# Performance work log

Hardware: AMD Instinct MI355X
Metric: run time of the kernel (lower is better)

The kernel has to match this reference:

```python
import jax, jax.numpy as jnp
import numpy as np

B, NS, NC, D = 32, 1024, 1024, 256   # batch, sentence len, comment len, latent/embedding dim
K = 128                              # co-attention latent size (self.k)
CLIP_R = 2.0
EPS = 1e-5

def _norm(x):
    return jnp.sqrt(jnp.maximum(jnp.sum(x * x, -1, keepdims=True), 1e-15))

def artanh(x):
    x = jnp.clip(x, -1 + 1e-5, 1 - 1e-5)
    return 0.5 * (jnp.log1p(x) - jnp.log1p(-x))

# ---------- Poincare ball, c = 1 ----------
def p_logmap0(y):
    yn = _norm(y)
    return artanh(yn) * y / yn

def p_expmap0(u):
    un = _norm(u)
    return jnp.tanh(un) * u / un

def mobius_add(x, y):
    xy = jnp.sum(x * y, -1, keepdims=True)
    x2 = jnp.sum(x * x, -1, keepdims=True)
    y2 = jnp.sum(y * y, -1, keepdims=True)
    num = (1 + 2 * xy + y2) * x + (1 - x2) * y
    den = jnp.maximum(1 + 2 * xy + x2 * y2, 1e-15)
    return num / den

def mobius_matvec(m, x):
    # geoopt convention: result = 'x @ m^T' transported through the ball
    xn = _norm(x)
    mx = jnp.matmul(x, jnp.swapaxes(m, -1, -2))
    mxn = _norm(mx)
    return jnp.tanh(mxn / xn * artanh(xn)) * mx / mxn

# ---------- Lorentz hyperboloid, k = 1 ----------
def l_expmap0_space(v_space):
    # exp map at origin of a tangent vector with zero time component
    vn = _norm(v_space)
    return jnp.concatenate([jnp.cosh(vn), jnp.sinh(vn) * v_space / vn], -1)

def euclid_to_lorentz(x):
    xn = _norm(x) + EPS
    x = x * jnp.minimum(1.0, CLIP_R / xn)  # clip_r feature clipping
    return l_expmap0_space(x)              # F.pad time=0 then expmap0

def lorentz_linear(x, W, b):
    y = jnp.matmul(x, W.T) + b
    space = y[..., 1:]
    time = jnp.sqrt(jnp.sum(space * space, -1, keepdims=True) + 1.0)
    return jnp.concatenate([time, space], -1)

def lorentz_act(x):
    space = jax.nn.gelu(x[..., 1:], approximate=False)
    time = jnp.sqrt(jnp.sum(space * space, -1, keepdims=True) + 1.0)
    return jnp.concatenate([time, space], -1)

def lorentz_to_poincare(x):
    return x[..., 1:] / (x[..., :1] + 1.0)

def l_inner(u, v):
    return -u[..., :1] * v[..., :1] + jnp.sum(u[..., 1:] * v[..., 1:], -1, keepdims=True)

def centroid(x, w):
    avg = jnp.matmul(w, x)  # weighted Lorentz average, then renormalize to hyperboloid
    den = jnp.sqrt(jnp.maximum(jnp.abs(l_inner(avg, avg)), 1e-8))
    return avg / den

def l_logmap0_space(x):
    t = jnp.maximum(x[..., :1], 1 + 1e-7)
    return jnp.arccosh(t) * x[..., 1:] / _norm(x[..., 1:])

def lorentz_concat(x, y):
    z = jnp.concatenate([l_logmap0_space(x), l_logmap0_space(y)], -1)
    return l_expmap0_space(z)


def setup_inputs() -> dict:
    key = jax.random.key(0)
    ks = jax.random.split(key, 8)
    sentence = jax.random.normal(ks[0], (B, NS, D), jnp.float32)
    comment = jax.random.normal(ks[1], (B, NC, D), jnp.float32)
    comment = 0.9 * comment / (_norm(comment) + 1.0)  # valid Poincare-ball points
    w = lambda k, o, i: jax.random.normal(k, (o, i), jnp.float32) * 0.05
    return {
        'sentence_rep': sentence,
        'comment_rep': comment,
        'Wl_W': w(ks[2], D + 1, D + 1), 'Wl_b': jnp.zeros((D + 1,), jnp.float32),
        'Wc_W': w(ks[3], K + 1, D + 1), 'Wc_b': jnp.zeros((K + 1,), jnp.float32),
        'Ws_W': w(ks[4], K + 1, D + 1), 'Ws_b': jnp.zeros((K + 1,), jnp.float32),
        'whs': jax.random.uniform(ks[5], (1, K), jnp.float32),
        'whc': jax.random.uniform(ks[6], (1, K), jnp.float32),
    }


def reference(sentence_rep, comment_rep, Wl_W, Wl_b, Wc_W, Wc_b, Ws_W, Ws_b, whs, whc):
    T = lambda a: jnp.swapaxes(a, -1, -2)
    # Fourier mixing (real part, as torch .float() on complex)
    s = jnp.fft.fft2(sentence_rep).real.astype(jnp.float32)
    c = jnp.fft.fft2(p_logmap0(comment_rep)).real.astype(jnp.float32)
    Ls = euclid_to_lorentz(s)            # [B,NS,D+1]
    Lc = euclid_to_lorentz(c)            # [B,NC,D+1]
    L = lorentz_linear(Lc, Wl_W, Wl_b)   # [B,NC,D+1]
    L = lorentz_act(jnp.einsum('bnd,bmd->bnm', Ls, L))  # [B,NS,NC] affinity
    # Ws(sentence) and Wc(comment) in Poincare coords (computed once; original recomputes)
    Hs_a = lorentz_to_poincare(lorentz_linear(Ls, Ws_W, Ws_b))  # [B,NS,K]
    Hc_a = lorentz_to_poincare(lorentz_linear(Lc, Wc_W, Wc_b))  # [B,NC,K]
    Hs_b = mobius_matvec(T(Hc_a), L)          # [B,NS,K]
    Hs = mobius_add(Hs_a, Hs_b)
    Hs = p_expmap0(jax.nn.gelu(p_logmap0(Hs), approximate=False))
    Hc_b = mobius_matvec(T(Hs_a), T(L))       # [B,NC,K]
    Hc = mobius_add(T(Hc_a), T(Hc_b))         # [B,K,NC]
    Hc = p_expmap0(jax.nn.gelu(p_logmap0(Hc), approximate=False))
    As = jax.nn.softmax(T(mobius_matvec(whs, Hs)), axis=-1)     # [B,1,NS]
    Ac = jax.nn.softmax(T(mobius_matvec(whc, T(Hc))), axis=-1)  # [B,1,NC]
    co_s = centroid(Ls, As)                   # [B,1,D+1]
    co_c = centroid(Lc, Ac)                   # [B,1,D+1]
    co_sc = jnp.squeeze(lorentz_concat(co_s, co_c), axis=1)     # [B,2D+1]
    return co_sc, As, Ac
```

## Files before the change

### kernel.cpp

```cpp
#include <hip/hip_runtime.h>
#include <cstdint>
#include <math.h>

#define NBATCH 32
#define NSQ 1024
#define NCQ 1024
#define DDIM 256
#define DP 257
#define KQ 128
#define KPAD 288
#define NFOLD 640
#define KF2 640
#define MXSPLIT 4194304

typedef __attribute__((ext_vector_type(8))) short short8;
typedef __attribute__((ext_vector_type(4))) float floatx4;

__device__ __forceinline__ float bf2f(ushort u) { return __uint_as_float(((uint)u) << 16); }
__device__ __forceinline__ ushort f2bf(float f) {
    uint u = __float_as_uint(f);
    return (ushort)((u + 0x7FFFu + ((u >> 16) & 1u)) >> 16);
}
__device__ __forceinline__ void gload16(const void* g, void* l) {
    __builtin_amdgcn_global_load_lds(
        (const __attribute__((address_space(1))) void*)g,
        (__attribute__((address_space(3))) void*)l,
        16, 0, 0);
}
__device__ __forceinline__ float artanh_clip(float x) {
    x = fminf(fmaxf(x, -1.0f + 1e-5f), 1.0f - 1e-5f);
    return 0.5f * (log1pf(x) - log1pf(-x));
}
__device__ __forceinline__ float gelu_f(float x) {
    return 0.5f * x * (1.0f + erff(x * 0.70710678118654752440f));
}
__device__ __forceinline__ float waveRedSum(float v) {
#pragma unroll
    for (int o = 32; o > 0; o >>= 1) v += __shfl_down(v, o, 64);
    return __shfl(v, 0, 64);
}
__device__ __forceinline__ void waveRedSum3(float& a, float& b, float& c) {
#pragma unroll
    for (int o = 32; o > 0; o >>= 1) {
        a += __shfl_down(a, o, 64);
        b += __shfl_down(b, o, 64);
        c += __shfl_down(c, o, 64);
    }
    a = __shfl(a, 0, 64); b = __shfl(b, 0, 64); c = __shfl(c, 0, 64);
}
__device__ __forceinline__ void waveRedSum2(float& a, float& b) {
#pragma unroll
    for (int o = 32; o > 0; o >>= 1) {
        a += __shfl_down(a, o, 64);
        b += __shfl_down(b, o, 64);
    }
    a = __shfl(a, 0, 64); b = __shfl(b, 0, 64);
}
__device__ __forceinline__ float blockRedSum(float v, float* buf) {
    int lane = threadIdx.x & 63, wid = threadIdx.x >> 6;
#pragma unroll
    for (int o = 32; o > 0; o >>= 1) v += __shfl_down(v, o, 64);
    __syncthreads();
    if (lane == 0) buf[wid] = v;
    __syncthreads();
    int nw = blockDim.x >> 6;
    float s = buf[0];
    for (int i = 1; i < nw; i++) s += buf[i];
    return s;
}
__device__ __forceinline__ float blockRedMax(float v, float* buf) {
    int lane = threadIdx.x & 63, wid = threadIdx.x >> 6;
#pragma unroll
    for (int o = 32; o > 0; o >>= 1) v = fmaxf(v, __shfl_down(v, o, 64));
    __syncthreads();
    if (lane == 0) buf[wid] = v;
    __syncthreads();
    int nw = blockDim.x >> 6;
    float s = buf[0];
    for (int i = 1; i < nw; i++) s = fmaxf(s, buf[i]);
    return s;
}

template <bool A_NN, bool B_NN, bool OUT_BF16, bool BIAS, bool ATOMIC, int NSPLIT, bool DUAL>
__global__ __launch_bounds__(256) void mfma_gemm(
    const short* __restrict__ A, int lda, int64_t sA,
    const short* __restrict__ B, int ldb, int64_t sB,
    void* __restrict__ Cv, int ldc, int64_t sC,
    const float* __restrict__ bias, int M, int N, int K,
    const short* __restrict__ A1, const short* __restrict__ B1, int64_t cOff1,
    const float* __restrict__ biasB)
{
    __shared__ short As[128][32];
    __shared__ short Bs[128][32];
    int bx = blockIdx.x, by = blockIdx.y, bz = blockIdx.z;
    {
        const int gx = gridDim.x, gy = gridDim.y;
        const int nblk = gx * gy * gridDim.z;
        if ((nblk & 7) == 0) {
            int flat = bx + gx * (by + gy * bz);
            int logical = (flat & 7) * (nblk >> 3) + (flat >> 3);
            bx = logical % gx; logical /= gx;
            by = logical % gy; bz = logical / gy;
        }
    }
    const int zz = bz;
    int zb, ks, half;
    if (DUAL) { half = zz & 1; zb = zz >> 1; ks = 0; }
    else      { zb = zz / NSPLIT; ks = zz - zb * NSPLIT; half = 0; }
    const short* Ap = (DUAL && half) ? A1 : A;
    const short* Bp = (DUAL && half) ? B1 : B;
    Ap += (int64_t)zb * sA;
    Bp += (int64_t)zb * sB;
    const int kper = K / NSPLIT;
    const int kbeg = ks * kper, kend = kbeg + kper;
    const int m0 = by * 128, n0 = bx * 128;
    const int t = threadIdx.x;
    const int lane = t & 63, w = t >> 6;
    const int wm = (w & 1) * 64, wn = (w >> 1) * 64;
    floatx4 acc[4][4] = {};
    for (int k0 = kbeg; k0 < kend; k0 += 32) {
        if (!A_NN) {
            int r = t >> 2, c8 = (t & 3) * 8;
            const short* ap = Ap + (int64_t)(m0 + r) * lda + k0 + c8;
            gload16(ap, &As[r][c8]);
            gload16(ap + (int64_t)64 * lda, &As[r + 64][c8]);
        } else {
            int r2 = t >> 4, c8 = (t & 15) * 8;
            int kk = 2 * r2;
            const ushort* a0 = (const ushort*)Ap + (int64_t)(k0 + kk) * lda + m0 + c8;
            uint4 v0 = *(const uint4*)a0;
            uint4 v1 = *(const uint4*)(a0 + lda);
            const ushort* p0 = (const ushort*)&v0;
            const ushort* p1 = (const ushort*)&v1;
#pragma unroll
            for (int i = 0; i < 8; i++) {
                uint pk = (uint)p0[i] | ((uint)p1[i] << 16);
                *(uint*)&As[c8 + i][kk] = pk;
            }
        }
        if (!B_NN) {
            int r = t >> 2, c8 = (t & 3) * 8;
            const short* bp = Bp + (int64_t)(n0 + r) * ldb + k0 + c8;
            gload16(bp, &Bs[r][c8]);
            gload16(bp + (int64_t)64 * ldb, &Bs[r + 64][c8]);
        } else {
            int r2 = t >> 4, c8 = (t & 15) * 8;
            int kk = 2 * r2;
            const ushort* b0 = (const ushort*)Bp + (int64_t)(k0 + kk) * ldb + n0 + c8;
            uint4 v0 = *(const uint4*)b0;
            uint4 v1 = *(const uint4*)(b0 + ldb);
            const ushort* p0 = (const ushort*)&v0;
            const ushort* p1 = (const ushort*)&v1;
#pragma unroll
            for (int i = 0; i < 8; i++) {
                uint pk = (uint)p0[i] | ((uint)p1[i] << 16);
                *(uint*)&Bs[c8 + i][kk] = pk;
            }
        }
        __syncthreads();
        short8 af[4], bfv[4];
#pragma unroll
        for (int i = 0; i < 4; i++)
            af[i] = *(const short8*)&As[wm + 16 * i + (lane & 15)][8 * (lane >> 4)];
#pragma unroll
        for (int i = 0; i < 4; i++)
            bfv[i] = *(const short8*)&Bs[wn + 16 * i + (lane & 15)][8 * (lane >> 4)];
#pragma unroll
        for (int i = 0; i < 4; i++)
#pragma unroll
            for (int j = 0; j < 4; j++)
                acc[i][j] = __builtin_amdgcn_mfma_f32_16x16x32_bf16(af[i], bfv[j], acc[i][j], 0, 0, 0);
        __syncthreads();
    }
    const int q = lane >> 4, c = lane & 15;
    int64_t cbase = (int64_t)zb * sC + ((DUAL && half) ? cOff1 : 0);
    if (NSPLIT > 1 && !ATOMIC) cbase += (int64_t)ks * cOff1;
    const float* bsel = (BIAS && biasB && zb) ? biasB : bias;
#pragma unroll
    for (int j = 0; j < 4; j++) {
        int col = n0 + wn + 16 * j + c;
        float bv = BIAS ? bsel[col] : 0.0f;
#pragma unroll
        for (int i = 0; i < 4; i++) {
            int rowb = m0 + wm + 16 * i + 4 * q;
#pragma unroll
            for (int r = 0; r < 4; r++) {
                float v = acc[i][j][r] + bv;
                int64_t idx = cbase + (int64_t)(rowb + r) * ldc + col;
                if (ATOMIC)       atomicAdd((float*)Cv + idx, v);
                else if (OUT_BF16) ((ushort*)Cv)[idx] = f2bf(v);
                else               ((float*)Cv)[idx] = v;
            }
        }
    }
}

__global__ __launch_bounds__(256) void genconst_kernel(
    ushort* CS1c, ushort* CS1s, ushort* C2, ushort* S2,
    const float* __restrict__ WlW, const float* __restrict__ WsW, const float* __restrict__ WcW,
    ushort* Wl, ushort* Ws, ushort* Wc)
{
    int blk = blockIdx.x, t = threadIdx.x;
    if (blk < 3200) {
        int idx = blk * 256 + t;
        int hs = idx >= 409600;
        int e = idx - hs * 409600;
        int n = e / KF2, k = e - n * KF2;
        float v = 0.0f;
        if (k <= 512) {
            int p = (n * k) & 1023;
            float ang = (6.28318530717958647692f / 1024.0f) * (float)p;
            v = hs ? ((k == 0) ? 0.0f : -sinf(ang)) : cosf(ang);
        }
        (hs ? CS1s : CS1c)[e] = f2bf(v);
    } else if (blk < 3456) {
        int idx = (blk - 3200) * 256 + t;
        int d = idx >> 8, j = idx & 255;
        int p = (d * j) & 255;
        float ang = (6.28318530717958647692f / 256.0f) * (float)p;
        C2[idx] = f2bf(cosf(ang));
        S2[idx] = f2bf(sinf(ang));
    } else {
        int r = blk - 3456;
        const float* src; ushort* dst; int srow;
        if (r < 256)      { src = WlW; dst = Wl + r * KPAD;        srow = r + 1; }
        else if (r < 384) { src = WsW; dst = Ws + (r - 256) * KPAD; srow = r - 256 + 1; }
        else              { src = WcW; dst = Wc + (r - 384) * KPAD; srow = r - 384 + 1; }
        dst[t] = (t < DP) ? f2bf(src[(int64_t)srow * DP + t]) : (ushort)0;
        if (t < KPAD - 256) {
            int t2 = t + 256;
            dst[t2] = (t2 < DP) ? f2bf(src[(int64_t)srow * DP + t2]) : (ushort)0;
        }
    }
}

__global__ __launch_bounds__(256) void prep_fold_kernel(const float* __restrict__ sent,
                                                        const float* __restrict__ comm,
                                                        ushort* __restrict__ XC, ushort* __restrict__ XS) {
    int bp = blockIdx.x;
    int z = blockIdx.y * 4 + (threadIdx.x >> 6);
    int lane = threadIdx.x & 63;
    int m2 = (1024 - bp) & 1023;
    const float* base = (z < 32) ? sent + (int64_t)z * 262144 : comm + (int64_t)(z - 32) * 262144;
    float4 a = *(const float4*)(base + bp * 256 + 4 * lane);
    float4 b = *(const float4*)(base + m2 * 256 + 4 * lane);
    if (z >= 32) {
        float s1 = a.x * a.x + a.y * a.y + a.z * a.z + a.w * a.w;
        float s2 = b.x * b.x + b.y * b.y + b.z * b.z + b.w * b.w;
        waveRedSum2(s1, s2);
        float yn1 = sqrtf(fmaxf(s1, 1e-15f));
        float f1 = artanh_clip(yn1) / yn1;
        a.x *= f1; a.y *= f1; a.z *= f1; a.w *= f1;
        float yn2 = sqrtf(fmaxf(s2, 1e-15f));
        float f2v = artanh_clip(yn2) / yn2;
        b.x *= f2v; b.y *= f2v; b.z *= f2v; b.w *= f2v;
    }
    int64_t o = ((int64_t)z * NFOLD + bp) * 256 + 4 * lane;
    bool single = (bp == 0) || (bp == 512);
    ushort4 oc;
    oc.x = f2bf(single ? a.x : a.x + b.x);
    oc.y = f2bf(single ? a.y : a.y + b.y);
    oc.z = f2bf(single ? a.z : a.z + b.z);
    oc.w = f2bf(single ? a.w : a.w + b.w);
    *(ushort4*)(XC + o) = oc;
    if (!single) {
        ushort4 os;
        os.x = f2bf(a.x - b.x); os.y = f2bf(a.y - b.y);
        os.z = f2bf(a.z - b.z); os.w = f2bf(a.w - b.w);
        *(ushort4*)(XS + o) = os;
    }
}

__global__ __launch_bounds__(256) void e2l_kernel(const ushort* __restrict__ YcYs,
                                                  ushort* __restrict__ Lsb, ushort* __restrict__ Lcb) {
    int64_t row = (int64_t)blockIdx.x * 4 + (threadIdx.x >> 6);
    int lane = threadIdx.x & 63;
    int z = (int)(row >> 10), n = (int)(row & 1023);
    int np = (n <= 512) ? n : 1024 - n;
    float sgn = (n <= 512) ? 1.0f : -1.0f;
    const ushort* base = YcYs + (int64_t)z * 327680 + np * 256 + 4 * lane;
    ushort4 uc = *(const ushort4*)base;
    ushort4 us = *(const ushort4*)(base + 163840);
    float v0 = bf2f(uc.x) + sgn * bf2f(us.x);
    float v1 = bf2f(uc.y) + sgn * bf2f(us.y);
    float v2 = bf2f(uc.z) + sgn * bf2f(us.z);
    float v3 = bf2f(uc.w) + sgn * bf2f(us.w);
    float s = waveRedSum(v0 * v0 + v1 * v1 + v2 * v2 + v3 * v3);
    float xn = sqrtf(fmaxf(s, 1e-15f)) + 1e-5f;
    float sc = fminf(1.0f, 2.0f / xn);
    float s2 = fmaxf(s * sc * sc, 1e-15f);
    float vn = sqrtf(s2);
    float e = expf(vn);
    float ei = 1.0f / e;
    float shv = (vn < 1e-4f) ? 1.0f : (e - ei) * 0.5f / vn;
    float fac = shv * sc;
    ushort* ob = (row < 32768 ? Lsb + row * KPAD : Lcb + (row - 32768) * KPAD);
    ob[1 + 4 * lane + 0] = f2bf(fac * v0);
    ob[1 + 4 * lane + 1] = f2bf(fac * v1);
    ob[1 + 4 * lane + 2] = f2bf(fac * v2);
    ob[1 + 4 * lane + 3] = f2bf(fac * v3);
    if (lane == 0) ob[0] = f2bf((e + ei) * 0.5f);
    if (lane < KPAD - DP) ob[DP + lane] = 0;
}

__global__ __launch_bounds__(256) void lnorm_kernel(ushort* __restrict__ Llin_bf) {
    int64_t row = (int64_t)blockIdx.x * 4 + (threadIdx.x >> 6);
    int lane = threadIdx.x & 63;
    ushort* ob = Llin_bf + row * KPAD;
    float s = 0.f;
#pragma unroll
    for (int i = 0; i < 4; i++) { float v = bf2f(ob[1 + 4 * lane + i]); s += v * v; }
    s = waveRedSum(s);
    if (lane == 0) ob[0] = f2bf(sqrtf(s + 1.0f));
    if (lane < KPAD - DP) ob[DP + lane] = 0;
}

__global__ __launch_bounds__(256) void poinc2_kernel(ushort* __restrict__ Hcat) {
    int64_t row = (int64_t)blockIdx.x * 4 + (threadIdx.x >> 6);
    int lane = threadIdx.x & 63;
    ushort* r = Hcat + row * KQ;
    ushort2 u = *(ushort2*)&r[2 * lane];
    float v0 = bf2f(u.x), v1 = bf2f(u.y);
    float s = waveRedSum(v0 * v0 + v1 * v1);
    float inv = 1.0f / (sqrtf(s + 1.0f) + 1.0f);
    ushort2 o; o.x = f2bf(v0 * inv); o.y = f2bf(v1 * inv);
    *(ushort2*)&r[2 * lane] = o;
}

__global__ __launch_bounds__(256) void tmat_kernel(ushort* __restrict__ inout, ushort* __restrict__ outp,
                                                   float* __restrict__ rowpart, float* __restrict__ colpart) {
    __shared__ ushort tile[64][68];
    int z = blockIdx.z;
    int r0 = blockIdx.x * 64, c0 = blockIdx.y * 64;
    ushort* ib = inout + (int64_t)z * 1048576;
    ushort* ob = outp + (int64_t)z * 1048576;
    int t = threadIdx.x;
    int row = t >> 2;
    int cq = (t & 3) * 8;
    {
        ushort* src = ib + (int64_t)(r0 + row) * 1024 + c0;
        float rsum = 0.f;
#pragma unroll
        for (int s = 0; s < 2; s++) {
            int cb = cq + 32 * s;
            uint4 v = *(const uint4*)(src + cb);
            ushort g[8];
            const ushort* pv = (const ushort*)&v;
#pragma unroll
            for (int k = 0; k < 8; k++) {
                g[k] = f2bf(gelu_f(bf2f(pv[k])));
                float fb = bf2f(g[k]);
                if (!(c0 == 0 && cb == 0 && k == 0)) rsum += fb * fb;
            }
            *(uint4*)(src + cb) = *(const uint4*)g;
            *(ushort4*)&tile[row][cb] = *(const ushort4*)&g[0];
            *(ushort4*)&tile[row][cb + 4] = *(const ushort4*)&g[4];
        }
        rsum += __shfl_xor(rsum, 1, 64);
        rsum += __shfl_xor(rsum, 2, 64);
        if ((t & 3) == 0)
            rowpart[((int64_t)(z * 16 + blockIdx.y)) * 1024 + r0 + row] = rsum;
    }
    __syncthreads();
    {
        int i2 = row;
        ushort* dst = ob + (int64_t)(c0 + i2) * 1024 + r0;
        float csum = 0.f;
#pragma unroll
        for (int s = 0; s < 2; s++) {
            int cb = cq + 32 * s;
            ushort g[8];
#pragma unroll
            for (int k = 0; k < 8; k++) {
                g[k] = tile[cb + k][i2];
                float a = bf2f(g[k]);
                csum += a * a;
            }
            *(uint4*)(dst + cb) = *(const uint4*)g;
        }
        csum += __shfl_xor(csum, 1, 64);
        csum += __shfl_xor(csum, 2, 64);
        if ((t & 3) == 0)
            colpart[((int64_t)(z * 16 + blockIdx.x)) * 1024 + c0 + i2] = csum;
    }
}

__global__ __launch_bounds__(256) void combine_kernel(
    const float* __restrict__ rowpart, const float* __restrict__ colpart,
    ushort* __restrict__ Lmat, ushort* __restrict__ LmatT,
    float* __restrict__ xnrow, float* __restrict__ colsum)
{
    __shared__ float red[4];
    int b = blockIdx.x, t = threadIdx.x;
    float t2 = 0.f;
#pragma unroll
    for (int i = 0; i < 4; i++) {
        int n = t + 256 * i;
        const float* rp = rowpart + (int64_t)b * 16384 + n;
        float s = 0.f;
#pragma unroll
        for (int c = 0; c < 16; c++) s += rp[c * 1024];
        float tim = sqrtf(1.0f + s);
        ushort tb = f2bf(tim);
        Lmat[((int64_t)(b * 1024 + n)) * 1024] = tb;
        LmatT[(int64_t)b * 1048576 + n] = tb;
        xnrow[b * 1024 + n] = sqrtf(fmaxf(1.0f + 2.0f * s, 1e-15f));
        t2 += tim * tim;
    }
#pragma unroll
    for (int i = 0; i < 4; i++) {
        int m = t + 256 * i;
        const float* cp = colpart + (int64_t)b * 16384 + m;
        float s = 0.f;
#pragma unroll
        for (int c = 0; c < 16; c++) s += cp[c * 1024];
        if (m > 0) colsum[b * 1024 + m] = s;
    }
    float tt = blockRedSum(t2, red);
    if (t == 0) colsum[b * 1024] = tt;
}

__global__ __launch_bounds__(256) void colfac_kernel(const float* __restrict__ colsum,
                                                     const float* __restrict__ mxcT,
                                                     float* __restrict__ fac_c) {
    int b = blockIdx.x; int m = blockIdx.y * 256 + threadIdx.x;
    float xn = sqrtf(fmaxf(colsum[b * NCQ + m], 1e-15f));
    const float* base = mxcT + (int64_t)b * KQ * NCQ + m;
    const float* base2 = base + MXSPLIT;
    float sm = 0.f;
    for (int j = 0; j < KQ; j++) {
        float v = base[j * NCQ] + base2[j * NCQ];
        sm += v * v;
    }
    float mxn = sqrtf(fmaxf(sm, 1e-15f));
    fac_c[b * NCQ + m] = tanhf(mxn / xn * artanh_clip(xn)) / mxn;
}

__global__ __launch_bounds__(256) void rowops_s_kernel(
    const ushort* __restrict__ Hsa, const float* __restrict__ mxs,
    const float* __restrict__ xnrow, const float* __restrict__ whs,
    float* __restrict__ logits)
{
    const int t = threadIdx.x;
    const int lane = t & 63;
    const int wid = t >> 6;
    const int sub = lane & 7;
    const int rg  = lane >> 3;
    const int64_t row = (int64_t)blockIdx.x * 32 + wid * 8 + rg;
    const ushort* p = Hsa + row * KQ + sub * 16;
    const float*  q = mxs + row * KQ + sub * 16;

    float pf[16], qf[16];
    {
        uint4 u0 = *(const uint4*)p;
        uint4 u1 = *(const uint4*)(p + 8);
        const ushort* pu0 = (const ushort*)&u0;
        const ushort* pu1 = (const ushort*)&u1;
#pragma unroll
        for (int i = 0; i < 8; i++) { pf[i] = bf2f(pu0[i]); pf[8 + i] = bf2f(pu1[i]); }
    }
#pragma unroll
    for (int i = 0; i < 16; i += 4) {
        float4 a  = *(const float4*)(q + i);
        float4 b2 = *(const float4*)(q + i + MXSPLIT);
        qf[i + 0] = a.x + b2.x; qf[i + 1] = a.y + b2.y;
        qf[i + 2] = a.z + b2.z; qf[i + 3] = a.w + b2.w;
    }
    float r1 = 0.f, r2 = 0.f, r3 = 0.f;
#pragma unroll
    for (int i = 0; i < 16; i++) {
        r1 += qf[i] * qf[i]; r2 += pf[i] * qf[i]; r3 += pf[i] * pf[i];
    }
#pragma unroll
    for (int o = 4; o > 0; o >>= 1) {
        r1 += __shfl_xor(r1, o, 64);
        r2 += __shfl_xor(r2, o, 64);
        r3 += __shfl_xor(r3, o, 64);
    }
    float mxn = sqrtf(fmaxf(r1, 1e-15f));
    float xn = xnrow[row];
    float fac = tanhf(mxn / xn * artanh_clip(xn)) / mxn;
    float xy = fac * r2;
    float x2 = r3;
    float y2 = fac * fac * r1;
    float ca = 1.f + 2.f * xy + y2, cb = 1.f - x2;
    float den = fmaxf(1.f + 2.f * xy + x2 * y2, 1e-15f);
    float hn2 = (ca * ca * x2 + 2.f * ca * cb * xy + cb * cb * y2) / (den * den);
    float hn = sqrtf(fmaxf(hn2, 1e-15f));
    float uf = artanh_clip(hn) / hn;
    float ufd = uf / den;
    float cbf = cb * fac;
    float wv[16];
#pragma unroll
    for (int i = 0; i < 16; i += 4) *(float4*)&wv[i] = *(const float4*)(whs + sub * 16 + i);
    float r4 = 0.f, r5 = 0.f;
#pragma unroll
    for (int i = 0; i < 16; i++) {
        float g = gelu_f(ufd * (ca * pf[i] + cbf * qf[i]));
        r4 += g * g;
        r5 += g * wv[i];
    }
#pragma unroll
    for (int o = 4; o > 0; o >>= 1) {
        r4 += __shfl_xor(r4, o, 64);
        r5 += __shfl_xor(r5, o, 64);
    }
    float gn = sqrtf(fmaxf(r4, 1e-15f));
    float ef = tanhf(gn) / gn;
    float dot = ef * r5;
    float Hn = sqrtf(fmaxf(ef * ef * r4, 1e-15f));
    float mxn2 = sqrtf(fmaxf(dot * dot, 1e-15f));
    float lg = tanhf(mxn2 / Hn * artanh_clip(Hn)) * dot / mxn2;
    if (sub == 0) logits[row] = lg;
}

__global__ void thsa_kernel(const ushort* __restrict__ in, ushort* __restrict__ outp) {
    __shared__ ushort tile[32][33];
    int z = blockIdx.z;
    int n0 = blockIdx.x * 32, j0 = blockIdx.y * 32;
    const ushort* ib = in + (int64_t)z * 131072;
    ushort* ob = outp + (int64_t)z * 131072;
    int tx = threadIdx.x, ty = threadIdx.y;
    for (int i = 0; i < 32; i += 8) tile[ty + i][tx] = ib[(n0 + ty + i) * 128 + j0 + tx];
    __syncthreads();
    for (int i = 0; i < 32; i += 8) ob[(j0 + ty + i) * 1024 + n0 + tx] = tile[tx][ty + i];
}

__global__ __launch_bounds__(256) void rowops_c_kernel(const ushort* __restrict__ HcAT,
                                                       float* __restrict__ mx,
                                                       const float* __restrict__ fac_c) {
    int64_t row = (int64_t)blockIdx.x * 4 + (threadIdx.x >> 6);
    int lane = threadIdx.x & 63;
    int b = (int)(row >> 7);
    const ushort* xb = HcAT + row * (int64_t)NCQ + 16 * lane;
    float* yb = mx + row * (int64_t)NCQ + 16 * lane;
    const float* fb = fac_c + b * NCQ + 16 * lane;
    float xv[16], yv[16];
    {
        uint4 u0 = *(const uint4*)xb;
        uint4 u1 = *(const uint4*)(xb + 8);
        const ushort* pu0 = (const ushort*)&u0;
        const ushort* pu1 = (const ushort*)&u1;
#pragma unroll
        for (int i = 0; i < 8; i++) { xv[i] = bf2f(pu0[i]); xv[8 + i] = bf2f(pu1[i]); }
    }
#pragma unroll
    for (int i = 0; i < 16; i += 4) {
        float4 v1 = *(const float4*)(yb + i);
        float4 v2 = *(const float4*)(yb + i + MXSPLIT);
        float4 fv = *(const float4*)(fb + i);
        yv[i + 0] = fv.x * (v1.x + v2.x);
        yv[i + 1] = fv.y * (v1.y + v2.y);
        yv[i + 2] = fv.z * (v1.z + v2.z);
        yv[i + 3] = fv.w * (v1.w + v2.w);
    }
    float xy = 0.f, x2 = 0.f, y2 = 0.f;
#pragma unroll
    for (int i = 0; i < 16; i++) { xy += xv[i] * yv[i]; x2 += xv[i] * xv[i]; y2 += yv[i] * yv[i]; }
    waveRedSum3(xy, x2, y2);
    float ca = 1.f + 2.f * xy + y2, cb = 1.f - x2;
    float den = fmaxf(1.f + 2.f * xy + x2 * y2, 1e-15f);
    float hn2 = (ca * ca * x2 + 2.f * ca * cb * xy + cb * cb * y2) / (den * den);
    float hn = sqrtf(fmaxf(hn2, 1e-15f));
    float uf = artanh_clip(hn) / hn;
    float g[16]; float gn2 = 0.f;
#pragma unroll
    for (int i = 0; i < 16; i++) {
        float h = (ca * xv[i] + cb * yv[i]) / den;
        g[i] = gelu_f(uf * h);
        gn2 += g[i] * g[i];
    }
    gn2 = waveRedSum(gn2);
    float gn = sqrtf(fmaxf(gn2, 1e-15f));
    float ef = tanhf(gn) / gn;
#pragma unroll
    for (int i = 0; i < 16; i += 4) {
        float4 o = {ef * g[i], ef * g[i + 1], ef * g[i + 2], ef * g[i + 3]};
        *(float4*)(yb + i) = o;
    }
}

__global__ __launch_bounds__(256) void logitsc_kernel(const float* __restrict__ Hc, const float* __restrict__ whc, float* __restrict__ lgc) {
    int b = blockIdx.x; int m = blockIdx.y * 256 + threadIdx.x;
    const float* base = Hc + (int64_t)b * KQ * NCQ + m;
    float s1 = 0.f, s2 = 0.f;
    for (int j = 0; j < KQ; j++) { float v = base[j * NCQ]; s1 += v * whc[j]; s2 += v * v; }
    float xn = sqrtf(fmaxf(s2, 1e-15f));
    float mxn = sqrtf(fmaxf(s1 * s1, 1e-15f));
    lgc[b * NCQ + m] = tanhf(mxn / xn * artanh_clip(xn)) * s1 / mxn;
}

__global__ __launch_bounds__(256) void softmax_kernel(const float* __restrict__ lg, float* __restrict__ outp) {
    __shared__ float red[4];
    int b = blockIdx.x; int t = threadIdx.x;
    const float* x = lg + b * 1024;
    float v[4]; float m = -1e30f;
#pragma unroll
    for (int i = 0; i < 4; i++) { v[i] = x[t + 256 * i]; m = fmaxf(m, v[i]); }
    m = blockRedMax(m, red);
    float s = 0.f;
#pragma unroll
    for (int i = 0; i < 4; i++) { v[i] = expf(v[i] - m); s += v[i]; }
    s = blockRedSum(s, red);
    float inv = 1.0f / s;
#pragma unroll
    for (int i = 0; i < 4; i++) outp[b * 1024 + t + 256 * i] = v[i] * inv;
}

__global__ __launch_bounds__(320) void centroidA_kernel(
    const ushort* __restrict__ Lsb, const ushort* __restrict__ Lcb,
    const float* __restrict__ As, const float* __restrict__ Ac,
    float* __restrict__ part)
{
    int b = blockIdx.x;
    int which = blockIdx.y;
    int chunk = blockIdx.z;
    const ushort* L = which ? Lcb : Lsb;
    const float* w = which ? Ac : As;
    int t = threadIdx.x;
    if (t >= DP) return;
    const ushort* Lb = L + (int64_t)b * NSQ * KPAD + (int64_t)chunk * 128 * KPAD + t;
    const float* wb = w + b * NSQ + chunk * 128;
    float s = 0.f;
    for (int n = 0; n < 128; n++) s += wb[n] * bf2f(Lb[(int64_t)n * KPAD]);
    part[((int64_t)((b * 2 + which) * 8 + chunk)) * 264 + t] = s;
}
__global__ __launch_bounds__(320) void centroidB_kernel(
    const float* __restrict__ part, float* __restrict__ co_s, float* __restrict__ co_c)
{
    int b = blockIdx.x;
    int which = blockIdx.y;
    int t = threadIdx.x;
    if (t >= DP) return;
    const float* p = part + (int64_t)(b * 2 + which) * 8 * 264 + t;
    float s = 0.f;
#pragma unroll
    for (int c = 0; c < 8; c++) s += p[c * 264];
    (which ? co_c : co_s)[b * DP + t] = s;
}

__global__ __launch_bounds__(256) void final_kernel(const float* __restrict__ co_s, const float* __restrict__ co_c, float* __restrict__ outp) {
    __shared__ float red[4];
    int b = blockIdx.x, t = threadIdx.x;
    float zmine[2];
    for (int w = 0; w < 2; w++) {
        const float* co = (w ? co_c : co_s) + b * DP;
        float at = co[0];
        float asp = co[1 + t];
        float ssp = blockRedSum(asp * asp, red);
        float li = ssp - at * at;
        float den = sqrtf(fmaxf(fabsf(li), 1e-8f));
        float xt = at / den, xsp = asp / den;
        float s2 = blockRedSum(xsp * xsp, red);
        float nrm = sqrtf(fmaxf(s2, 1e-15f));
        float ac = acoshf(fmaxf(xt, 1.0f + 1e-7f));
        zmine[w] = ac * xsp / nrm;
    }
    float vn2 = blockRedSum(zmine[0] * zmine[0] + zmine[1] * zmine[1], red);
    float vn = sqrtf(fmaxf(vn2, 1e-15f));
    float sc = sinhf(vn) / vn;
    if (t == 0) outp[b * 513] = coshf(vn);
    outp[b * 513 + 1 + t] = sc * zmine[0];
    outp[b * 513 + 1 + 256 + t] = sc * zmine[1];
}

extern "C" void kernel_launch(void* const* d_in, const int* in_sizes, int n_in,
                              void* d_out, int out_size, void* d_ws, size_t ws_size,
                              hipStream_t stream)
{
    const float* sent = (const float*)d_in[0];
    const float* comm = (const float*)d_in[1];
    const float* WlW  = (const float*)d_in[2];
    const float* Wlb  = (const float*)d_in[3];
    const float* WcW  = (const float*)d_in[4];
    const float* Wcb  = (const float*)d_in[5];
    const float* WsW  = (const float*)d_in[6];
    const float* Wsb  = (const float*)d_in[7];
    const float* whs  = (const float*)d_in[8];
    const float* whc  = (const float*)d_in[9];
    float* out = (float*)d_out;
    (void)in_sizes; (void)n_in; (void)out_size; (void)ws_size;

    float* ws = (float*)d_ws;
    size_t off = 0;
    auto take = [&](size_t n) { float* p = ws + off; off += n; return p; };
    float*  xnrow = take(32768);
    float*  fac_c = take(32768);
    float*  lgs   = take(32768);
    float*  lgc   = take(32768);
    float*  co_s  = take(8224);
    float*  co_c  = take(8224);
    ushort* Ls_bf = (ushort*)take(4718592);
    ushort* Lc_bf = (ushort*)take(4718592);
    ushort* Wl_bf = (ushort*)take(36864);
    ushort* Ws_bf = (ushort*)take(18432);
    ushort* Wc_bf = (ushort*)take(18432);
    ushort* HsA_bf = (ushort*)take(2097152);
    ushort* HcA_bf = (ushort*)take(2097152);
    float*  part_cn   = take(1048576);
    float*  part_cent = take(135168);
    ushort* LmatT_bf  = (ushort*)take(16777216);
    float*  F     = take(33554432);

    ushort* XC_bf   = (ushort*)F;
    ushort* XS_bf   = (ushort*)(F + 5242880);
    ushort* Ff_bf   = (ushort*)(F + 10485760);
    ushort* CS1c    = (ushort*)(F + 20971520);
    ushort* CS1s    = (ushort*)(F + 21176320);
    ushort* C2_bf   = (ushort*)(F + 21381120);
    ushort* S2_bf   = (ushort*)(F + 21413888);
    ushort* YcYs    = (ushort*)F;
    ushort* Lmat_bf = (ushort*)F;
    ushort* Llin_bf = (ushort*)(F + 29360128);
    float*  mx      = F + 16777216;
    ushort* HsAT    = (ushort*)(F + 25165824);
    ushort* HcAT    = (ushort*)(F + 27262976);
    float*  colpart = F + 29360128;
    float*  colsum  = F + 30408704;

    float* AsOut = out + 16416;
    float* AcOut = out + 16416 + 32768;

    dim3 blk(256);
    const short* NUL = nullptr;

    genconst_kernel<<<3968, 256, 0, stream>>>(CS1c, CS1s, C2_bf, S2_bf, WlW, WsW, WcW, Wl_bf, Ws_bf, Wc_bf);

    prep_fold_kernel<<<dim3(513, 16), blk, 0, stream>>>(sent, comm, XC_bf, XS_bf);
    mfma_gemm<false,false,true,false,false,1,true><<<dim3(5,2,128), blk, 0, stream>>>(
        (const short*)C2_bf,256,0, (const short*)XC_bf,256,(int64_t)NFOLD*256, Ff_bf,1280,(int64_t)256*1280,
        nullptr, 256,NFOLD,256, (const short*)S2_bf, (const short*)XS_bf, 640, nullptr);
    mfma_gemm<false,false,true,false,false,1,true><<<dim3(2,5,128), blk, 0, stream>>>(
        (const short*)CS1c,KF2,0, (const short*)Ff_bf,1280,(int64_t)256*1280, YcYs,256,327680,
        nullptr, NFOLD,256,544, (const short*)CS1s, (const short*)(Ff_bf+640), 163840, nullptr);
    e2l_kernel<<<16384, blk, 0, stream>>>(YcYs, Ls_bf, Lc_bf);

    mfma_gemm<false,false,true,true,false,1,false><<<dim3(2,256,1), blk, 0, stream>>>(
        (const short*)Lc_bf,KPAD,0, (const short*)Wl_bf,KPAD,0, (void*)(Llin_bf+1),KPAD,0,
        Wlb+1, 32768,256,KPAD, NUL, NUL, 0, nullptr);
    lnorm_kernel<<<8192, blk, 0, stream>>>(Llin_bf);

    mfma_gemm<false,false,true,false,false,1,false><<<dim3(8,8,32), blk, 0, stream>>>(
        (const short*)Ls_bf,KPAD,294912, (const short*)Llin_bf,KPAD,294912, Lmat_bf,1024,1048576,
        nullptr, 1024,1024,KPAD, NUL, NUL, 0, nullptr);
    tmat_kernel<<<dim3(16,16,32), blk, 0, stream>>>(Lmat_bf, LmatT_bf, part_cn, colpart);
    combine_kernel<<<32, blk, 0, stream>>>(part_cn, colpart, Lmat_bf, LmatT_bf, xnrow, colsum);

    mfma_gemm<false,false,true,true,false,1,false><<<dim3(1,256,2), blk, 0, stream>>>(
        (const short*)Ls_bf,KPAD,9437184, (const short*)Ws_bf,KPAD,36864, HsA_bf,128,4194304,
        Wsb+1, 32768,128,KPAD, NUL, NUL, 0, Wcb+1);
    poinc2_kernel<<<16384, blk, 0, stream>>>(HsA_bf);

    thsa_kernel<<<dim3(32,4,64), dim3(32,8), 0, stream>>>(HsA_bf, HsAT);

    mfma_gemm<false,false,false,false,false,2,false><<<dim3(1,8,64), blk, 0, stream>>>(
        (const short*)Lmat_bf,1024,1048576, (const short*)HcAT,1024,131072, mx,128,131072,
        nullptr, 1024,128,1024, NUL, NUL, MXSPLIT, nullptr);
    rowops_s_kernel<<<1024, blk, 0, stream>>>(HsA_bf, mx, xnrow, whs, lgs);

    mfma_gemm<false,false,false,false,false,2,false><<<dim3(8,1,64), blk, 0, stream>>>(
        (const short*)HsAT,1024,131072, (const short*)LmatT_bf,1024,1048576, mx,1024,131072,
        nullptr, 128,1024,1024, NUL, NUL, MXSPLIT, nullptr);
    colfac_kernel<<<dim3(32,4), blk, 0, stream>>>(colsum, mx, fac_c);
    rowops_c_kernel<<<1024, blk, 0, stream>>>(HcAT, mx, fac_c);
    logitsc_kernel<<<dim3(32,4), blk, 0, stream>>>(mx, whc, lgc);

    softmax_kernel<<<64, blk, 0, stream>>>(lgs, AsOut);
    centroidA_kernel<<<dim3(32,2,8), 320, 0, stream>>>(Ls_bf, Lc_bf, AsOut, AcOut, part_cent);
    centroidB_kernel<<<dim3(32,2), 320, 0, stream>>>(part_cent, co_s, co_c);
    final_kernel<<<32, blk, 0, stream>>>(co_s, co_c, out);
}
```

Before: 468.0 us.

## Process two K-slices per barrier in GEMM and table-drive DFT constant generation

The MFMA GEMM now stages two 32-wide K tiles into separate LDS buffers before a single barrier pair and runs both MFMA batches. This halves barrier count per K step and gives more loads in flight, at the cost of doubled LDS per block, which may reduce occupancy. The unused NN transpose-load paths are removed. Constant generation now precomputes a 1024-entry cos/sin table once and uses lookups in restructured per-row blocks instead of per-element sinf/cosf across thousands of blocks.

```diff
diff --git a/kernel.cpp b/kernel.cpp
--- a/kernel.cpp
+++ b/kernel.cpp
@@ -81,7 +81,7 @@
     return s;
 }
 
-template <bool A_NN, bool B_NN, bool OUT_BF16, bool BIAS, bool ATOMIC, int NSPLIT, bool DUAL>
+template <bool OUT_BF16, bool BIAS, bool ATOMIC, int NSPLIT, bool DUAL>
 __global__ __launch_bounds__(256) void mfma_gemm(
     const short* __restrict__ A, int lda, int64_t sA,
     const short* __restrict__ B, int ldb, int64_t sB,
@@ -90,8 +90,10 @@
     const short* __restrict__ A1, const short* __restrict__ B1, int64_t cOff1,
     const float* __restrict__ biasB)
 {
-    __shared__ short As[128][32];
-    __shared__ short Bs[128][32];
+    __shared__ short As0[128][32];
+    __shared__ short Bs0[128][32];
+    __shared__ short As1[128][32];
+    __shared__ short Bs1[128][32];
     int bx = blockIdx.x, by = blockIdx.y, bz = blockIdx.z;
     {
         const int gx = gridDim.x, gy = gridDim.y;
@@ -117,61 +119,50 @@
     const int t = threadIdx.x;
     const int lane = t & 63, w = t >> 6;
     const int wm = (w & 1) * 64, wn = (w >> 1) * 64;
+    const int sr = t >> 2, sc8 = (t & 3) * 8;
     floatx4 acc[4][4] = {};
-    for (int k0 = kbeg; k0 < kend; k0 += 32) {
-        if (!A_NN) {
-            int r = t >> 2, c8 = (t & 3) * 8;
-            const short* ap = Ap + (int64_t)(m0 + r) * lda + k0 + c8;
-            gload16(ap, &As[r][c8]);
-            gload16(ap + (int64_t)64 * lda, &As[r + 64][c8]);
-        } else {
-            int r2 = t >> 4, c8 = (t & 15) * 8;
-            int kk = 2 * r2;
-            const ushort* a0 = (const ushort*)Ap + (int64_t)(k0 + kk) * lda + m0 + c8;
-            uint4 v0 = *(const uint4*)a0;
-            uint4 v1 = *(const uint4*)(a0 + lda);
-            const ushort* p0 = (const ushort*)&v0;
-            const ushort* p1 = (const ushort*)&v1;
-#pragma unroll
-            for (int i = 0; i < 8; i++) {
-                uint pk = (uint)p0[i] | ((uint)p1[i] << 16);
-                *(uint*)&As[c8 + i][kk] = pk;
-            }
-        }
-        if (!B_NN) {
-            int r = t >> 2, c8 = (t & 3) * 8;
-            const short* bp = Bp + (int64_t)(n0 + r) * ldb + k0 + c8;
-            gload16(bp, &Bs[r][c8]);
-            gload16(bp + (int64_t)64 * ldb, &Bs[r + 64][c8]);
-        } else {
-            int r2 = t >> 4, c8 = (t & 15) * 8;
-            int kk = 2 * r2;
-            const ushort* b0 = (const ushort*)Bp + (int64_t)(k0 + kk) * ldb + n0 + c8;
-            uint4 v0 = *(const uint4*)b0;
-            uint4 v1 = *(const uint4*)(b0 + ldb);
-            const ushort* p0 = (const ushort*)&v0;
-            const ushort* p1 = (const ushort*)&v1;
-#pragma unroll
-            for (int i = 0; i < 8; i++) {
-                uint pk = (uint)p0[i] | ((uint)p1[i] << 16);
-                *(uint*)&Bs[c8 + i][kk] = pk;
-            }
-        }
-        __syncthreads();
+
+    auto stageA = [&](short (*S)[32], int kk) {
+        const short* ap = Ap + (int64_t)(m0 + sr) * lda + kk + sc8;
+        gload16(ap, &S[sr][sc8]);
+        gload16(ap + (int64_t)64 * lda, &S[sr + 64][sc8]);
+    };
+    auto stageB = [&](short (*S)[32], int kk) {
+        const short* bp = Bp + (int64_t)(n0 + sr) * ldb + kk + sc8;
+        gload16(bp, &S[sr][sc8]);
+        gload16(bp + (int64_t)64 * ldb, &S[sr + 64][sc8]);
+    };
+    auto domfma = [&](short (*SA)[32], short (*SB)[32]) {
         short8 af[4], bfv[4];
 #pragma unroll
         for (int i = 0; i < 4; i++)
-            af[i] = *(const short8*)&As[wm + 16 * i + (lane & 15)][8 * (lane >> 4)];
+            af[i] = *(const short8*)&SA[wm + 16 * i + (lane & 15)][8 * (lane >> 4)];
 #pragma unroll
         for (int i = 0; i < 4; i++)
-            bfv[i] = *(const short8*)&Bs[wn + 16 * i + (lane & 15)][8 * (lane >> 4)];
+            bfv[i] = *(const short8*)&SB[wn + 16 * i + (lane & 15)][8 * (lane >> 4)];
 #pragma unroll
         for (int i = 0; i < 4; i++)
 #pragma unroll
             for (int j = 0; j < 4; j++)
                 acc[i][j] = __builtin_amdgcn_mfma_f32_16x16x32_bf16(af[i], bfv[j], acc[i][j], 0, 0, 0);
+    };
+
+    int k0 = kbeg;
+    for (; k0 + 64 <= kend; k0 += 64) {
+        stageA(As0, k0);       stageB(Bs0, k0);
+        stageA(As1, k0 + 32);  stageB(Bs1, k0 + 32);
         __syncthreads();
-    }
+        domfma(As0, Bs0);
+        domfma(As1, Bs1);
+        __syncthreads();
+    }
+    if (k0 < kend) {
+        stageA(As0, k0);      stageB(Bs0, k0);
+        __syncthreads();
+        domfma(As0, Bs0);
+        __syncthreads();
+    }
+
     const int q = lane >> 4, c = lane & 15;
     int64_t cbase = (int64_t)zb * sC + ((DUAL && half) ? cOff1 : 0);
     if (NSPLIT > 1 && !ATOMIC) cbase += (int64_t)ks * cOff1;
@@ -195,33 +186,49 @@
     }
 }
 
+__global__ __launch_bounds__(256) void trigtab_kernel(float* __restrict__ tab) {
+    int p = blockIdx.x * 256 + threadIdx.x;
+    float ang = (6.28318530717958647692f / 1024.0f) * (float)p;
+    tab[p] = cosf(ang);
+    tab[1024 + p] = sinf(ang);
+}
+
 __global__ __launch_bounds__(256) void genconst_kernel(
+    const float* __restrict__ tab,
     ushort* CS1c, ushort* CS1s, ushort* C2, ushort* S2,
     const float* __restrict__ WlW, const float* __restrict__ WsW, const float* __restrict__ WcW,
     ushort* Wl, ushort* Ws, ushort* Wc)
 {
+    __shared__ float lct[1024], lst[1024];
     int blk = blockIdx.x, t = threadIdx.x;
-    if (blk < 3200) {
-        int idx = blk * 256 + t;
-        int hs = idx >= 409600;
-        int e = idx - hs * 409600;
-        int n = e / KF2, k = e - n * KF2;
-        float v = 0.0f;
-        if (k <= 512) {
-            int p = (n * k) & 1023;
-            float ang = (6.28318530717958647692f / 1024.0f) * (float)p;
-            v = hs ? ((k == 0) ? 0.0f : -sinf(ang)) : cosf(ang);
+    if (blk < 704) {
+        for (int i = t; i < 1024; i += 256) { lct[i] = tab[i]; lst[i] = tab[1024 + i]; }
+        __syncthreads();
+    }
+    if (blk < 640) {
+        int n = blk;
+        for (int k = t; k < 544; k += 256) {
+            float vc, vs;
+            if (k <= 512) {
+                int p = (n * k) & 1023;
+                vc = lct[p];
+                vs = (k == 0) ? 0.0f : -lst[p];
+            } else { vc = 0.0f; vs = 0.0f; }
+            CS1c[n * KF2 + k] = f2bf(vc);
+            CS1s[n * KF2 + k] = f2bf(vs);
         }
-        (hs ? CS1s : CS1c)[e] = f2bf(v);
-    } else if (blk < 3456) {
-        int idx = (blk - 3200) * 256 + t;
-        int d = idx >> 8, j = idx & 255;
-        int p = (d * j) & 255;
-        float ang = (6.28318530717958647692f / 256.0f) * (float)p;
-        C2[idx] = f2bf(cosf(ang));
-        S2[idx] = f2bf(sinf(ang));
+    } else if (blk < 704) {
+        int base = (blk - 640) * 1024;
+#pragma unroll
+        for (int i = 0; i < 4; i++) {
+            int idx = base + t + 256 * i;
+            int d = idx >> 8, j = idx & 255;
+            int p = ((d * j) & 255) << 2;
+            C2[idx] = f2bf(lct[p]);
+            S2[idx] = f2bf(lst[p]);
+        }
     } else {
-        int r = blk - 3456;
+        int r = blk - 704;
         const float* src; ushort* dst; int srow;
         if (r < 256)      { src = WlW; dst = Wl + r * KPAD;        srow = r + 1; }
         else if (r < 384) { src = WsW; dst = Ws + (r - 256) * KPAD; srow = r - 256 + 1; }
@@ -690,6 +697,7 @@
     float*  lgc   = take(32768);
     float*  co_s  = take(8224);
     float*  co_c  = take(8224);
+    float*  trigtab = take(2048);
     ushort* Ls_bf = (ushort*)take(4718592);
     ushort* Lc_bf = (ushort*)take(4718592);
     ushort* Wl_bf = (ushort*)take(36864);
@@ -724,41 +732,43 @@
     dim3 blk(256);
     const short* NUL = nullptr;
 
-    genconst_kernel<<<3968, 256, 0, stream>>>(CS1c, CS1s, C2_bf, S2_bf, WlW, WsW, WcW, Wl_bf, Ws_bf, Wc_bf);
+    trigtab_kernel<<<4, 256, 0, stream>>>(trigtab);
+    genconst_kernel<<<1216, 256, 0, stream>>>(trigtab, CS1c, CS1s, C2_bf, S2_bf,
+                                              WlW, WsW, WcW, Wl_bf, Ws_bf, Wc_bf);
 
     prep_fold_kernel<<<dim3(513, 16), blk, 0, stream>>>(sent, comm, XC_bf, XS_bf);
-    mfma_gemm<false,false,true,false,false,1,true><<<dim3(5,2,128), blk, 0, stream>>>(
+    mfma_gemm<true,false,false,1,true><<<dim3(5,2,128), blk, 0, stream>>>(
         (const short*)C2_bf,256,0, (const short*)XC_bf,256,(int64_t)NFOLD*256, Ff_bf,1280,(int64_t)256*1280,
         nullptr, 256,NFOLD,256, (const short*)S2_bf, (const short*)XS_bf, 640, nullptr);
-    mfma_gemm<false,false,true,false,false,1,true><<<dim3(2,5,128), blk, 0, stream>>>(
+    mfma_gemm<true,false,false,1,true><<<dim3(2,5,128), blk, 0, stream>>>(
         (const short*)CS1c,KF2,0, (const short*)Ff_bf,1280,(int64_t)256*1280, YcYs,256,327680,
         nullptr, NFOLD,256,544, (const short*)CS1s, (const short*)(Ff_bf+640), 163840, nullptr);
     e2l_kernel<<<16384, blk, 0, stream>>>(YcYs, Ls_bf, Lc_bf);
 
-    mfma_gemm<false,false,true,true,false,1,false><<<dim3(2,256,1), blk, 0, stream>>>(
+    mfma_gemm<true,true,false,1,false><<<dim3(2,256,1), blk, 0, stream>>>(
         (const short*)Lc_bf,KPAD,0, (const short*)Wl_bf,KPAD,0, (void*)(Llin_bf+1),KPAD,0,
         Wlb+1, 32768,256,KPAD, NUL, NUL, 0, nullptr);
     lnorm_kernel<<<8192, blk, 0, stream>>>(Llin_bf);
 
-    mfma_gemm<false,false,true,false,false,1,false><<<dim3(8,8,32), blk, 0, stream>>>(
+    mfma_gemm<true,false,false,1,false><<<dim3(8,8,32), blk, 0, stream>>>(
         (const short*)Ls_bf,KPAD,294912, (const short*)Llin_bf,KPAD,294912, Lmat_bf,1024,1048576,
         nullptr, 1024,1024,KPAD, NUL, NUL, 0, nullptr);
     tmat_kernel<<<dim3(16,16,32), blk, 0, stream>>>(Lmat_bf, LmatT_bf, part_cn, colpart);
     combine_kernel<<<32, blk, 0, stream>>>(part_cn, colpart, Lmat_bf, LmatT_bf, xnrow, colsum);
 
-    mfma_gemm<false,false,true,true,false,1,false><<<dim3(1,256,2), blk, 0, stream>>>(
+    mfma_gemm<true,true,false,1,false><<<dim3(1,256,2), blk, 0, stream>>>(
         (const short*)Ls_bf,KPAD,9437184, (const short*)Ws_bf,KPAD,36864, HsA_bf,128,4194304,
         Wsb+1, 32768,128,KPAD, NUL, NUL, 0, Wcb+1);
     poinc2_kernel<<<16384, blk, 0, stream>>>(HsA_bf);
 
     thsa_kernel<<<dim3(32,4,64), dim3(32,8), 0, stream>>>(HsA_bf, HsAT);
 
-    mfma_gemm<false,false,false,false,false,2,false><<<dim3(1,8,64), blk, 0, stream>>>(
+    mfma_gemm<false,false,false,2,false><<<dim3(1,8,64), blk, 0, stream>>>(
         (const short*)Lmat_bf,1024,1048576, (const short*)HcAT,1024,131072, mx,128,131072,
         nullptr, 1024,128,1024, NUL, NUL, MXSPLIT, nullptr);
     rowops_s_kernel<<<1024, blk, 0, stream>>>(HsA_bf, mx, xnrow, whs, lgs);
 
-    mfma_gemm<false,false,false,false,false,2,false><<<dim3(8,1,64), blk, 0, stream>>>(
+    mfma_gemm<false,false,false,2,false><<<dim3(8,1,64), blk, 0, stream>>>(
         (const short*)HsAT,1024,131072, (const short*)LmatT_bf,1024,1048576, mx,1024,131072,
         nullptr, 128,1024,1024, NUL, NUL, MXSPLIT, nullptr);
     colfac_kernel<<<dim3(32,4), blk, 0, stream>>>(colsum, mx, fac_c);
```

After: 465.6 us. Within noise of the previous version (-0.5%).
